# Optimization experiments

Hardware: AMD Instinct MI355X
Metric: run time of the kernel (lower is better)

## Reference

```python
import jax, jax.numpy as jnp
import numpy as np

B, C, T, N, P = 32, 32, 8192, 256, 6  # batch, num_chars, text_len, n_neurons, pattern_lens


def conv2d_valid(x, w):
    # x: (B, C, T, 1) NHWC; w: (C, P, 1, N) HWIO -> out (B, 1, T-P+1, N)
    return jax.lax.conv_general_dilated(
        x, w, window_strides=(1, 1), padding='VALID',
        dimension_numbers=('NHWC', 'HWIO', 'NHWC'))


def setup_inputs() -> dict:
    key = jax.random.key(0)
    k1, k2 = jax.random.split(key)
    chars = jax.random.randint(k1, (B, T), 0, C)
    # one-hot encoded character text: (B, C, T, 1)
    input_ = jax.nn.one_hot(chars, C, axis=1, dtype=jnp.float32)[..., None]
    patterns = jax.random.uniform(k2, (C, P, 1, N), dtype=jnp.float32)
    return {"input_": input_, "patterns": patterns}


def reference(input_, patterns):
    # Discretize patterns: per (position, neuron), 1.0 at the argmax char iff column sum > 0
    pmax = jnp.max(patterns, axis=0, keepdims=True)
    psum = jnp.sum(patterns, axis=0, keepdims=True)
    patterns_discrete = ((patterns == pmax) & (psum > 0)).astype(jnp.float32)  # (C,P,1,N)

    conv = conv2d_valid(input_, patterns_discrete)            # (B, 1, T-P+1, N)
    t_len = input_.shape[2]
    conv = jnp.pad(conv, ((0, 0), (0, 0), (0, t_len - conv.shape[2]), (0, 0)))  # pad to (B,1,T,N)

    pattern_sums = jnp.sum(patterns_discrete, axis=(0, 1))    # (1, N)
    # exact-match indicator: conv value equals number of active pattern positions
    final = (conv[:, 0] == pattern_sums[0]).astype(jnp.float32)  # (B, T, N)
    return jnp.transpose(final, (0, 2, 1))[..., None]            # (B, N, T, 1)
```

## Files before the change

### kernel.cpp

```cpp
#include <hip/hip_runtime.h>

#define B_ 32
#define C_ 32
#define T_ 8192
#define N_ 256
#define P_ 6
#define TV_ (T_ - P_ + 1)

__global__ void k_disc(const float* __restrict__ pat, unsigned* __restrict__ tabs) {
    int tid = blockIdx.x * blockDim.x + threadIdx.x;
    if (tid >= P_ * N_) return;
    int p = tid / N_;
    int n = tid - p * N_;
    float maxv = -3.402823466e+38f;
    float sum = 0.0f;
    unsigned mask = 0u;
    #pragma unroll
    for (int c = 0; c < C_; ++c) {
        float v = pat[((size_t)c * P_ + p) * N_ + n];
        sum += v;
        if (v > maxv) { maxv = v; mask = (1u << c); }
        else if (v == maxv) { mask |= (1u << c); }
    }
    if (!(sum > 0.0f)) mask = 0u;
    int pc = __popc(mask);
    unsigned req = (unsigned)(__ffs((int)mask) - 1);
    unsigned xs = (pc == 1) ? req * 0x01010101u : 0x7F7F7F7Fu;
    unsigned om = (pc == 0) ? 0u : 0x80808080u;
    tabs[n * 12 + p]     = xs;
    tabs[n * 12 + 6 + p] = om;
}

__global__ void k_chars(const float* __restrict__ inp, unsigned* __restrict__ chars32) {
    int bx = blockIdx.x;
    int b  = bx >> 3;
    int t  = ((bx & 7) << 10) + (threadIdx.x << 2);
    const float* base = inp + (size_t)b * C_ * T_ + t;
    float ax = 0.f, ay = 0.f, az = 0.f, aw = 0.f;
    #pragma unroll
    for (int c = 0; c < C_; ++c) {
        float4 v = *(const float4*)(base + (size_t)c * T_);
        float fc = (float)c;
        ax += fc * v.x; ay += fc * v.y; az += fc * v.z; aw += fc * v.w;
    }
    unsigned w = ((unsigned)(ax + 0.5f))
               | ((unsigned)(ay + 0.5f) << 8)
               | ((unsigned)(az + 0.5f) << 16)
               | ((unsigned)(aw + 0.5f) << 24);
    chars32[((size_t)b * T_ + t) >> 2] = w;
}

__global__ void k_final(const unsigned char* __restrict__ chars,
                        const unsigned* __restrict__ tabs,
                        float* __restrict__ out) {
    __shared__ unsigned s32[258];
    int tc  = blockIdx.x;
    int ng  = blockIdx.y;
    int b   = blockIdx.z;
    int tid = threadIdx.x;
    int t0  = tc << 10;
    int tb  = t0 + (tid << 2);

    const unsigned* csrc = (const unsigned*)(chars + (size_t)b * T_ + t0);
    s32[tid] = csrc[tid];
    if (tid < 2) {
        unsigned v = 0u;
        int gt = t0 + 1024 + tid * 4;
        if (gt < T_) v = csrc[256 + tid];
        s32[256 + tid] = v;
    }
    __syncthreads();

    unsigned w0 = s32[tid], w1 = s32[tid + 1], w2 = s32[tid + 2];
    unsigned cw0 = w0;
    unsigned cw1 = __builtin_amdgcn_alignbyte(w1, w0, 1);
    unsigned cw2 = __builtin_amdgcn_alignbyte(w1, w0, 2);
    unsigned cw3 = __builtin_amdgcn_alignbyte(w1, w0, 3);
    unsigned cw4 = w1;
    unsigned cw5 = __builtin_amdgcn_alignbyte(w2, w1, 1);

    int n0 = ng << 5;
    const uint4* tp = (const uint4*)tabs + (size_t)n0 * 3;
    float* obase = out + ((size_t)(b * N_ + n0)) * T_ + tb;
    bool tail = (tc == 7) && (tb + 3 >= TV_);

    #pragma unroll 4
    for (int g = 0; g < 32; ++g) {
        uint4 A = tp[g * 3 + 0];
        uint4 Bv = tp[g * 3 + 1];
        uint4 Cv = tp[g * 3 + 2];

        unsigned orv;
        orv  = ((cw0 ^ A.x)  + 0x7F7F7F7FU) & Bv.z;
        orv |= ((cw1 ^ A.y)  + 0x7F7F7F7FU) & Bv.w;
        orv |= ((cw2 ^ A.z)  + 0x7F7F7F7FU) & Cv.x;
        orv |= ((cw3 ^ A.w)  + 0x7F7F7F7FU) & Cv.y;
        orv |= ((cw4 ^ Bv.x) + 0x7F7F7F7FU) & Cv.z;
        orv |= ((cw5 ^ Bv.y) + 0x7F7F7F7FU) & Cv.w;

        float res[4];
        #pragma unroll
        for (int j = 0; j < 4; ++j)
            res[j] = (orv & (0x80u << (8 * j))) ? 0.0f : 1.0f;

        if (tail) {
            unsigned act = Bv.z | Bv.w | Cv.x | Cv.y | Cv.z | Cv.w;
            float padf = (act == 0u) ? 1.0f : 0.0f;
            #pragma unroll
            for (int j = 0; j < 4; ++j)
                if (tb + j >= TV_) res[j] = padf;
        }

        float4 r; r.x = res[0]; r.y = res[1]; r.z = res[2]; r.w = res[3];
        *(float4*)(obase + (size_t)g * T_) = r;
    }
}

extern "C" void kernel_launch(void* const* d_in, const int* in_sizes, int n_in,
                              void* d_out, int out_size, void* d_ws, size_t ws_size,
                              hipStream_t stream) {
    const float* input_   = (const float*)d_in[0];
    const float* patterns = (const float*)d_in[1];
    float* out = (float*)d_out;

    unsigned*      tabs  = (unsigned*)d_ws;
    unsigned char* chars = (unsigned char*)d_ws + 16384;

    hipLaunchKernelGGL(k_disc, dim3((P_ * N_ + 255) / 256), dim3(256), 0, stream,
                       patterns, tabs);
    hipLaunchKernelGGL(k_chars, dim3(B_ * (T_ / 1024)), dim3(256), 0, stream,
                       input_, (unsigned*)chars);
    hipLaunchKernelGGL(k_final, dim3(T_ / 1024, N_ / 32, B_), dim3(256), 0, stream,
                       chars, tabs, out);
}
```

Before: 68.65 us.

## Fuse char decoding into output kernel and cover all neurons per block

Merges the character-decoding kernel into the final match kernel. Each block now decodes its own one-hot slice, plus a two-word halo, straight into shared memory instead of reading a byte buffer from workspace. The grid drops the neuron-group dimension, so each block loops over all 256 neurons. This removes one kernel launch and the workspace round trip for the chars, but the grid shrinks to 256 blocks of 4 waves each, which may limit latency hiding on the large store-bound output write.

Result: slower. 110.4 us (+60.8%).

```diff
diff --git a/kernel.cpp b/kernel.cpp
--- a/kernel.cpp
+++ b/kernel.cpp
@@ -31,43 +31,47 @@
     tabs[n * 12 + 6 + p] = om;
 }
 
-__global__ void k_chars(const float* __restrict__ inp, unsigned* __restrict__ chars32) {
-    int bx = blockIdx.x;
-    int b  = bx >> 3;
-    int t  = ((bx & 7) << 10) + (threadIdx.x << 2);
-    const float* base = inp + (size_t)b * C_ * T_ + t;
-    float ax = 0.f, ay = 0.f, az = 0.f, aw = 0.f;
-    #pragma unroll
-    for (int c = 0; c < C_; ++c) {
-        float4 v = *(const float4*)(base + (size_t)c * T_);
-        float fc = (float)c;
-        ax += fc * v.x; ay += fc * v.y; az += fc * v.z; aw += fc * v.w;
-    }
-    unsigned w = ((unsigned)(ax + 0.5f))
-               | ((unsigned)(ay + 0.5f) << 8)
-               | ((unsigned)(az + 0.5f) << 16)
-               | ((unsigned)(aw + 0.5f) << 24);
-    chars32[((size_t)b * T_ + t) >> 2] = w;
-}
-
-__global__ void k_final(const unsigned char* __restrict__ chars,
-                        const unsigned* __restrict__ tabs,
-                        float* __restrict__ out) {
+__global__ void k_mega(const float* __restrict__ inp,
+                       const unsigned* __restrict__ tabs,
+                       float* __restrict__ out) {
     __shared__ unsigned s32[258];
     int tc  = blockIdx.x;
-    int ng  = blockIdx.y;
-    int b   = blockIdx.z;
+    int b   = blockIdx.y;
     int tid = threadIdx.x;
     int t0  = tc << 10;
     int tb  = t0 + (tid << 2);
 
-    const unsigned* csrc = (const unsigned*)(chars + (size_t)b * T_ + t0);
-    s32[tid] = csrc[tid];
-    if (tid < 2) {
-        unsigned v = 0u;
-        int gt = t0 + 1024 + tid * 4;
-        if (gt < T_) v = csrc[256 + tid];
-        s32[256 + tid] = v;
+    {
+        const float* base = inp + (size_t)b * C_ * T_ + tb;
+        float ax = 0.f, ay = 0.f, az = 0.f, aw = 0.f;
+        #pragma unroll
+        for (int c = 0; c < C_; ++c) {
+            float4 v = *(const float4*)(base + (size_t)c * T_);
+            float fc = (float)c;
+            ax += fc * v.x; ay += fc * v.y; az += fc * v.z; aw += fc * v.w;
+        }
+        s32[tid] = ((unsigned)(ax + 0.5f))
+                 | ((unsigned)(ay + 0.5f) << 8)
+                 | ((unsigned)(az + 0.5f) << 16)
+                 | ((unsigned)(aw + 0.5f) << 24);
+        if (tid < 2) {
+            unsigned w = 0u;
+            if (tc < 7) {
+                const float* hb = inp + (size_t)b * C_ * T_ + (t0 + 1024 + (tid << 2));
+                float hx = 0.f, hy = 0.f, hz = 0.f, hw = 0.f;
+                #pragma unroll
+                for (int c = 0; c < C_; ++c) {
+                    float4 v = *(const float4*)(hb + (size_t)c * T_);
+                    float fc = (float)c;
+                    hx += fc * v.x; hy += fc * v.y; hz += fc * v.z; hw += fc * v.w;
+                }
+                w = ((unsigned)(hx + 0.5f))
+                  | ((unsigned)(hy + 0.5f) << 8)
+                  | ((unsigned)(hz + 0.5f) << 16)
+                  | ((unsigned)(hw + 0.5f) << 24);
+            }
+            s32[256 + tid] = w;
+        }
     }
     __syncthreads();
 
@@ -79,14 +83,13 @@
     unsigned cw4 = w1;
     unsigned cw5 = __builtin_amdgcn_alignbyte(w2, w1, 1);
 
-    int n0 = ng << 5;
-    const uint4* tp = (const uint4*)tabs + (size_t)n0 * 3;
-    float* obase = out + ((size_t)(b * N_ + n0)) * T_ + tb;
+    const uint4* tp = (const uint4*)tabs;
+    float* obase = out + (size_t)b * N_ * T_ + tb;
     bool tail = (tc == 7) && (tb + 3 >= TV_);
 
     #pragma unroll 4
-    for (int g = 0; g < 32; ++g) {
-        uint4 A = tp[g * 3 + 0];
+    for (int g = 0; g < N_; ++g) {
+        uint4 A  = tp[g * 3 + 0];
         uint4 Bv = tp[g * 3 + 1];
         uint4 Cv = tp[g * 3 + 2];
 
@@ -123,13 +126,10 @@
     const float* patterns = (const float*)d_in[1];
     float* out = (float*)d_out;
 
-    unsigned*      tabs  = (unsigned*)d_ws;
-    unsigned char* chars = (unsigned char*)d_ws + 16384;
+    unsigned* tabs = (unsigned*)d_ws;
 
     hipLaunchKernelGGL(k_disc, dim3((P_ * N_ + 255) / 256), dim3(256), 0, stream,
                        patterns, tabs);
-    hipLaunchKernelGGL(k_chars, dim3(B_ * (T_ / 1024)), dim3(256), 0, stream,
-                       input_, (unsigned*)chars);
-    hipLaunchKernelGGL(k_final, dim3(T_ / 1024, N_ / 32, B_), dim3(256), 0, stream,
-                       chars, tabs, out);
+    hipLaunchKernelGGL(k_mega, dim3(T_ / 1024, B_), dim3(256), 0, stream,
+                       input_, tabs, out);
 }
```
